# Kernel tuning notes

Measured on AMD Instinct MI355X. Metric: run time of the kernel, lower is better.

## Reference

```python
import jax, jax.numpy as jnp
import numpy as np

D = 512
M_FUT = 3
EPS = 1e-12


def _lin(x, W, b):
    return x @ W + b


def _svd_orthogonalize(m):
    # m: [B, 9] -> [B, 3, 3] SO(3) via SVD orthogonalization (special Procrustes)
    m = m.reshape(-1, 3, 3)
    norm = jnp.maximum(jnp.linalg.norm(m, axis=-1, keepdims=True), EPS)
    mt = jnp.swapaxes(m / norm, -1, -2)          # normalize rows, then transpose
    u, s, vh = jnp.linalg.svd(mt, full_matrices=False)
    v = jnp.swapaxes(vh, -1, -2)                 # torch.svd returns V, jax returns V^H
    ut = jnp.swapaxes(u, -1, -2)
    det = jnp.linalg.det(jnp.matmul(v, ut))      # [B]
    v_adj = jnp.concatenate([v[:, :, :-1], v[:, :, -1:] * det[:, None, None]], axis=2)
    return jnp.matmul(v_adj, ut)


def setup_inputs() -> dict:
    key = jax.random.key(0)
    ks = iter(jax.random.split(key, 40))
    B, N, M = 32, 3, M_FUT
    ph = pw = 37
    BN, hw = B * N, ph * pw
    sc = 1.0 / np.sqrt(D)
    rn = lambda *shape: (jax.random.normal(next(ks), shape, dtype=jnp.float32) * sc)
    inp = {
        'feat': jax.random.normal(next(ks), (BN, hw, D), dtype=jnp.float32),
        'patch_h': ph, 'patch_w': pw, 'batch_size': B, 'num_current_frames': N,
        # two ResConvBlocks, three 512x512 Linears each (in==out -> skip is identity)
        'W_res': rn(2, 3, D, D), 'b_res': rn(2, 3, D),
        # TemporalCameraMLP
        'W_cur1': rn(D, D), 'b_cur1': rn(D), 'W_cur2': rn(D, D), 'b_cur2': rn(D),
        'W_tp1': rn(D, D), 'b_tp1': rn(D), 'W_tp2': rn(D, D * M), 'b_tp2': rn(D * M),
        'W_fut1': rn(D, D), 'b_fut1': rn(D), 'W_fut2': rn(D, D), 'b_fut2': rn(D),
        # more_mlps
        'W_m1': rn(D, D), 'b_m1': rn(D), 'W_m2': rn(D, D), 'b_m2': rn(D),
        # pose heads (fp32)
        'W_t': rn(D, 3), 'b_t': rn(3), 'W_r': rn(D, 9), 'b_r': rn(9),
    }
    return inp


def reference(feat, patch_h, patch_w, batch_size, num_current_frames,
              W_res, b_res, W_cur1, b_cur1, W_cur2, b_cur2,
              W_tp1, b_tp1, W_tp2, b_tp2, W_fut1, b_fut1, W_fut2, b_fut2,
              W_m1, b_m1, W_m2, b_m2, W_t, b_t, W_r, b_r):
    B, N = batch_size, num_current_frames
    M = W_tp2.shape[1] // W_tp2.shape[0]
    # stacked residual 1x1-conv (Linear) blocks
    for i in range(2):
        x = jax.nn.relu(_lin(feat, W_res[i, 0], b_res[i, 0]))
        x = jax.nn.relu(_lin(x, W_res[i, 1], b_res[i, 1]))
        x = jax.nn.relu(_lin(x, W_res[i, 2], b_res[i, 2]))
        feat = feat + x
    # AdaptiveAvgPool2d(1) over patch grid == mean over hw
    pooled = feat.mean(axis=1)                                  # [BN, D]
    # TemporalCameraMLP
    cur = _lin(jax.nn.relu(_lin(pooled, W_cur1, b_cur1)), W_cur2, b_cur2)   # [BN, D]
    gctx = pooled.reshape(B, N, -1).mean(axis=1)                            # [B, D]
    tf = _lin(jax.nn.relu(_lin(gctx, W_tp1, b_tp1)), W_tp2, b_tp2)          # [B, D*M]
    tf = tf.reshape(B * M, -1)
    fut = _lin(jax.nn.relu(_lin(tf, W_fut1, b_fut1)), W_fut2, b_fut2)       # [B*M, D]
    allf = jnp.concatenate([cur, fut], axis=0)                              # [B*(N+M), D]
    h = jax.nn.relu(_lin(jax.nn.relu(_lin(allf, W_m1, b_m1)), W_m2, b_m2))
    # pose head in fp32
    hf = h.astype(jnp.float32)
    out_t = _lin(hf, W_t, b_t)                                  # [newBN, 3]
    out_r = _lin(hf, W_r, b_r)                                  # [newBN, 9]
    r = _svd_orthogonalize(out_r)                               # [newBN, 3, 3]
    newBN = allf.shape[0]
    pose = jnp.zeros((newBN, 4, 4), dtype=jnp.float32)
    pose = pose.at[:, :3, :3].set(r)
    pose = pose.at[:, :3, 3].set(out_t)
    pose = pose.at[:, 3, 3].set(1.0)
    return pose
```

## Files before the change

kernel.cpp:

```cpp
#include <hip/hip_runtime.h>


typedef unsigned short u16;
typedef __attribute__((ext_vector_type(8))) short short8;
typedef __attribute__((ext_vector_type(4))) float f32x4;

constexpr int  DDIM    = 512;
constexpr long R_ROWS  = 96L * 1369L;
constexpr long R_PAD   = 2054L * 64L;

__device__ __forceinline__ u16 f2b(float f) {
  union { float f; unsigned u; } x; x.f = f;
  unsigned r = (x.u + 0x7FFFu + ((x.u >> 16) & 1u)) >> 16;
  return (u16)r;
}
__device__ __forceinline__ float b2f(u16 b) {
  union { unsigned u; float f; } x; x.u = ((unsigned)b) << 16;
  return x.f;
}

__global__ void convert_feat_k(const float* __restrict__ in, u16* __restrict__ out) {
  long i4 = ((long)blockIdx.x * 256 + threadIdx.x) * 4;
  if (i4 >= R_PAD * DDIM) return;
  ushort4 o;
  if (i4 < R_ROWS * DDIM) {
    float4 v = *(const float4*)(in + i4);
    o.x = f2b(v.x); o.y = f2b(v.y); o.z = f2b(v.z); o.w = f2b(v.w);
  } else {
    o.x = 0; o.y = 0; o.z = 0; o.w = 0;
  }
  *(ushort4*)(out + i4) = o;
}

__global__ void transpose_w_k(const float* __restrict__ W, u16* __restrict__ Wt) {
  int idx = blockIdx.x * 256 + threadIdx.x;
  if (idx >= 6 * 512 * 512) return;
  int g = idx >> 18, rem = idx & 262143;
  int n = rem >> 9, k = rem & 511;
  Wt[idx] = f2b(W[(long)g * 262144 + (long)k * 512 + n]);
}

__global__ __launch_bounds__(512, 2)
void fused_res_k(u16* __restrict__ A, const u16* __restrict__ Wt3,
                 const float* __restrict__ bias3) {
  __shared__ __align__(16) u16 S[64 * 512];
  float* S32 = (float*)S;
  const int tid  = threadIdx.x;
  const int lane = tid & 63;
  const int wn   = tid >> 6;
  const int l15  = lane & 15;
  const int quad = lane >> 4;
  const long rowBase = (long)blockIdx.x * 64;

#pragma unroll
  for (int j = 0; j < 8; ++j) {
    int L = tid + 512 * j;
    int r = L >> 6, cS = L & 63;
    int c = cS ^ (r & 7);
    const u16* ga = A + (rowBase + r) * DDIM + c * 8;
    __builtin_amdgcn_global_load_lds(
        (const __attribute__((address_space(1))) void*)ga,
        (__attribute__((address_space(3))) void*)&S[L * 8], 16, 0, 0);
  }
  __syncthreads();

  for (int layer = 0; layer < 3; ++layer) {
    const u16*  W    = Wt3 + (long)layer * 262144;
    const float* bias = bias3 + layer * 512;

    f32x4 acc[4][4];
#pragma unroll
    for (int i = 0; i < 4; ++i)
#pragma unroll
      for (int j = 0; j < 4; ++j) acc[i][j] = (f32x4){0.f, 0.f, 0.f, 0.f};

    const u16* wb = W + (long)(wn * 64 + l15) * DDIM + quad * 8;
    short8 bf[4], bfN[4];
#pragma unroll
    for (int j = 0; j < 4; ++j) bf[j] = *(const short8*)(wb + j * 16 * DDIM);

#pragma unroll
    for (int kk = 0; kk < 16; ++kk) {
      if (kk < 15) {
#pragma unroll
        for (int j = 0; j < 4; ++j)
          bfN[j] = *(const short8*)(wb + j * 16 * DDIM + (kk + 1) * 32);
      }
      short8 af[4];
      const int slot = ((kk * 4 + quad) ^ (l15 & 7)) * 8;
#pragma unroll
      for (int i = 0; i < 4; ++i)
        af[i] = *(const short8*)&S[(i * 16 + l15) * DDIM + slot];
#pragma unroll
      for (int i = 0; i < 4; ++i)
#pragma unroll
        for (int j = 0; j < 4; ++j)
          acc[i][j] = __builtin_amdgcn_mfma_f32_16x16x32_bf16(af[i], bf[j], acc[i][j], 0, 0, 0);
      if (kk < 15) {
#pragma unroll
        for (int j = 0; j < 4; ++j) bf[j] = bfN[j];
      }
    }

    __syncthreads();

    float bv[4];
#pragma unroll
    for (int j = 0; j < 4; ++j) bv[j] = bias[wn * 64 + j * 16 + l15];

    if (layer < 2) {
#pragma unroll
      for (int i = 0; i < 4; ++i)
#pragma unroll
        for (int j = 0; j < 4; ++j) {
          int col = wn * 64 + j * 16 + l15;
#pragma unroll
          for (int r = 0; r < 4; ++r) {
            int row = i * 16 + quad * 4 + r;
            float v = fmaxf(acc[i][j][r] + bv[j], 0.f);
            S[row * DDIM + (((col >> 3) ^ (row & 7)) << 3) + (col & 7)] = f2b(v);
          }
        }
      __syncthreads();
    } else {
#pragma unroll
      for (int h = 0; h < 2; ++h) {
#pragma unroll
        for (int i2 = 0; i2 < 2; ++i2) {
          int i = h * 2 + i2;
#pragma unroll
          for (int j = 0; j < 4; ++j) {
            int col = wn * 64 + j * 16 + l15;
#pragma unroll
            for (int r = 0; r < 4; ++r) {
              int row = i * 16 + quad * 4 + r;
              int rl  = row - h * 32;
              float v = fmaxf(acc[i][j][r] + bv[j], 0.f);
              S32[rl * DDIM + (((col >> 2) ^ (rl & 7)) << 2) + (col & 3)] = v;
            }
          }
        }
        __syncthreads();
#pragma unroll
        for (int it = 0; it < 4; ++it) {
          int idx = it * 512 + tid;
          int r = idx >> 6, c = idx & 63;
          float4 va = *(const float4*)&S32[r * DDIM + ((((2 * c)     ^ (r & 7))) << 2)];
          float4 vb = *(const float4*)&S32[r * DDIM + ((((2 * c + 1) ^ (r & 7))) << 2)];
          long g = (rowBase + h * 32 + r) * DDIM + c * 8;
          short8 xv = *(const short8*)&A[g];
          float vv[8] = {va.x, va.y, va.z, va.w, vb.x, vb.y, vb.z, vb.w};
          short8 o;
#pragma unroll
          for (int k = 0; k < 8; ++k) o[k] = (short)f2b(vv[k] + b2f((u16)xv[k]));
          *(short8*)&A[g] = o;
        }
        __syncthreads();
      }
    }
  }
}

__global__ void zero_k(float* p, int n) {
  int i = blockIdx.x * 256 + threadIdx.x;
  if (i < n) p[i] = 0.f;
}

__global__ void pool_k(const u16* __restrict__ feat, float* __restrict__ pooled) {
  int bn = blockIdx.x, ch = blockIdx.y, d = threadIdx.x;
  int p0 = ch * 172, p1 = p0 + 172;
  if (p1 > 1369) p1 = 1369;
  float s = 0.f;
  long base = ((long)bn * 1369 + p0) * DDIM + d;
  for (int p = p0; p < p1; ++p) { s += b2f(feat[base]); base += DDIM; }
  atomicAdd(&pooled[bn * DDIM + d], s * (1.0f / 1369.0f));
}

__global__ void gctx_k(const float* __restrict__ pooled, float* __restrict__ gctx) {
  int i = blockIdx.x * 256 + threadIdx.x;
  if (i >= 32 * DDIM) return;
  int b = i >> 9, d = i & 511;
  const float* p = pooled + (long)b * 3 * DDIM + d;
  gctx[i] = (p[0] + p[DDIM] + p[2 * DDIM]) * (1.0f / 3.0f);
}

template <bool RELU>
__global__ void lin_k(const float* __restrict__ in, const float* __restrict__ W,
                      const float* __restrict__ bias, float* __restrict__ out,
                      int K, int N) {
  int n = blockIdx.x * 256 + threadIdx.x;
  int r = blockIdx.y;
  if (n >= N) return;
  float acc = bias[n];
  const float* xi = in + (long)r * K;
#pragma unroll 8
  for (int k = 0; k < K; ++k) acc = fmaf(xi[k], W[(long)k * N + n], acc);
  if (RELU) acc = fmaxf(acc, 0.f);
  out[(long)r * N + n] = acc;
}

__global__ void pose_k(const float* __restrict__ h,
                       const float* __restrict__ Wt, const float* __restrict__ bt,
                       const float* __restrict__ Wr, const float* __restrict__ br,
                       float* __restrict__ out) {
  int row = blockIdx.x;
  int lane = threadIdx.x;
  const float* hr = h + (long)row * DDIM;
  float part[12];
#pragma unroll
  for (int c = 0; c < 12; ++c) {
    float acc = 0.f;
    for (int k = lane; k < DDIM; k += 64) {
      float wvv = (c < 3) ? Wt[k * 3 + c] : Wr[k * 9 + (c - 3)];
      acc += hr[k] * wvv;
    }
#pragma unroll
    for (int off = 32; off > 0; off >>= 1) acc += __shfl_down(acc, off);
    part[c] = acc;
  }
  if (lane != 0) return;

  double t3[3];
  for (int i = 0; i < 3; ++i) t3[i] = (double)part[i] + (double)bt[i];
  double m[3][3];
  for (int i = 0; i < 3; ++i)
    for (int j = 0; j < 3; ++j) m[i][j] = (double)part[3 + i * 3 + j] + (double)br[i * 3 + j];
  for (int i = 0; i < 3; ++i) {
    double nn = sqrt(m[i][0] * m[i][0] + m[i][1] * m[i][1] + m[i][2] * m[i][2]);
    if (nn < 1e-12) nn = 1e-12;
    m[i][0] /= nn; m[i][1] /= nn; m[i][2] /= nn;
  }
  double Km[3][3];
  for (int a = 0; a < 3; ++a)
    for (int b = 0; b < 3; ++b) {
      double s = 0;
      for (int i = 0; i < 3; ++i) s += m[i][a] * m[i][b];
      Km[a][b] = s;
    }
  double V[3][3] = {{1, 0, 0}, {0, 1, 0}, {0, 0, 1}};
  const int PQ[3][2] = {{0, 1}, {0, 2}, {1, 2}};
  for (int sweep = 0; sweep < 20; ++sweep) {
    for (int e = 0; e < 3; ++e) {
      int p = PQ[e][0], q = PQ[e][1];
      double apq = Km[p][q];
      if (apq == 0.0) continue;
      double tau = (Km[q][q] - Km[p][p]) / (2.0 * apq);
      double tt = (tau >= 0.0 ? 1.0 : -1.0) / (fabs(tau) + sqrt(1.0 + tau * tau));
      double cc = 1.0 / sqrt(1.0 + tt * tt), ss = tt * cc;
      for (int k = 0; k < 3; ++k) { double a1 = Km[p][k], a2 = Km[q][k]; Km[p][k] = cc * a1 - ss * a2; Km[q][k] = ss * a1 + cc * a2; }
      for (int k = 0; k < 3; ++k) { double a1 = Km[k][p], a2 = Km[k][q]; Km[k][p] = cc * a1 - ss * a2; Km[k][q] = ss * a1 + cc * a2; }
      for (int k = 0; k < 3; ++k) { double a1 = V[k][p], a2 = V[k][q]; V[k][p] = cc * a1 - ss * a2; V[k][q] = ss * a1 + cc * a2; }
    }
  }
  double lam[3] = {Km[0][0], Km[1][1], Km[2][2]};
  int o0 = 0, o1 = 1, o2 = 2; double detV = 1.0;
  if (lam[o0] < lam[o1]) { int t = o0; o0 = o1; o1 = t; detV = -detV; }
  if (lam[o1] < lam[o2]) { int t = o1; o1 = o2; o2 = t; detV = -detV; }
  if (lam[o0] < lam[o1]) { int t = o0; o0 = o1; o1 = t; detV = -detV; }
  double v0[3] = {V[0][o0], V[1][o0], V[2][o0]};
  double v1[3] = {V[0][o1], V[1][o1], V[2][o1]};
  double v2[3] = {V[0][o2], V[1][o2], V[2][o2]};
  double u0[3], u1[3];
  for (int i = 0; i < 3; ++i) u0[i] = m[i][0] * v0[0] + m[i][1] * v0[1] + m[i][2] * v0[2];
  double n0 = sqrt(u0[0] * u0[0] + u0[1] * u0[1] + u0[2] * u0[2]); if (n0 < 1e-30) n0 = 1e-30;
  for (int i = 0; i < 3; ++i) u0[i] /= n0;
  for (int i = 0; i < 3; ++i) u1[i] = m[i][0] * v1[0] + m[i][1] * v1[1] + m[i][2] * v1[2];
  double d01 = u0[0] * u1[0] + u0[1] * u1[1] + u0[2] * u1[2];
  for (int i = 0; i < 3; ++i) u1[i] -= d01 * u0[i];
  double n1 = sqrt(u1[0] * u1[0] + u1[1] * u1[1] + u1[2] * u1[2]); if (n1 < 1e-30) n1 = 1e-30;
  for (int i = 0; i < 3; ++i) u1[i] /= n1;
  double u2[3] = {u0[1] * u1[2] - u0[2] * u1[1],
                  u0[2] * u1[0] - u0[0] * u1[2],
                  u0[0] * u1[1] - u0[1] * u1[0]};
  float* o = out + (long)row * 16;
  for (int i = 0; i < 3; ++i) {
    for (int j = 0; j < 3; ++j)
      o[i * 4 + j] = (float)(u0[i] * v0[j] + u1[i] * v1[j] + detV * u2[i] * v2[j]);
    o[i * 4 + 3] = (float)t3[i];
  }
  o[12] = 0.f; o[13] = 0.f; o[14] = 0.f; o[15] = 1.f;
}

extern "C" void kernel_launch(void* const* d_in, const int* in_sizes, int n_in,
                              void* d_out, int out_size, void* d_ws, size_t ws_size,
                              hipStream_t stream) {
  (void)in_sizes; (void)n_in; (void)out_size; (void)ws_size;
  const float* feat   = (const float*)d_in[0];
  const float* W_res  = (const float*)d_in[5];
  const float* b_res  = (const float*)d_in[6];
  const float* W_cur1 = (const float*)d_in[7];
  const float* b_cur1 = (const float*)d_in[8];
  const float* W_cur2 = (const float*)d_in[9];
  const float* b_cur2 = (const float*)d_in[10];
  const float* W_tp1  = (const float*)d_in[11];
  const float* b_tp1  = (const float*)d_in[12];
  const float* W_tp2  = (const float*)d_in[13];
  const float* b_tp2  = (const float*)d_in[14];
  const float* W_fut1 = (const float*)d_in[15];
  const float* b_fut1 = (const float*)d_in[16];
  const float* W_fut2 = (const float*)d_in[17];
  const float* b_fut2 = (const float*)d_in[18];
  const float* W_m1   = (const float*)d_in[19];
  const float* b_m1   = (const float*)d_in[20];
  const float* W_m2   = (const float*)d_in[21];
  const float* b_m2   = (const float*)d_in[22];
  const float* W_t    = (const float*)d_in[23];
  const float* b_t    = (const float*)d_in[24];
  const float* W_r    = (const float*)d_in[25];
  const float* b_r    = (const float*)d_in[26];

  char* ws = (char*)d_ws;
  const size_t SZ_BIG = (size_t)R_PAD * DDIM * 2;
  u16* A   = (u16*)(ws);
  u16* Wt6 = (u16*)(ws + 3 * SZ_BIG);
  char* tail = ws + 3 * SZ_BIG + (size_t)6 * 512 * 512 * 2;
  float* pooled = (float*)(tail);
  float* gctx   = pooled + 96 * 512;
  float* tmp    = gctx + 32 * 512;
  float* tfb    = tmp + 192 * 512;
  float* allf   = tfb + 32 * 1536;
  float* h2     = allf + 192 * 512;
  float* outp   = (float*)d_out;

  convert_feat_k<<<65728, 256, 0, stream>>>(feat, A);
  transpose_w_k<<<6144, 256, 0, stream>>>(W_res, Wt6);

  const size_t WS1 = (size_t)512 * 512;
  fused_res_k<<<2054, 512, 0, stream>>>(A, Wt6,           b_res);
  fused_res_k<<<2054, 512, 0, stream>>>(A, Wt6 + 3 * WS1, b_res + 3 * 512);

  zero_k<<<(96 * 512 + 255) / 256, 256, 0, stream>>>(pooled, 96 * 512);
  pool_k<<<dim3(96, 8), 512, 0, stream>>>(A, pooled);
  gctx_k<<<(32 * 512 + 255) / 256, 256, 0, stream>>>(pooled, gctx);

  lin_k<true ><<<dim3(2, 96),  256, 0, stream>>>(pooled, W_cur1, b_cur1, tmp, 512, 512);
  lin_k<false><<<dim3(2, 96),  256, 0, stream>>>(tmp, W_cur2, b_cur2, allf, 512, 512);
  lin_k<true ><<<dim3(2, 32),  256, 0, stream>>>(gctx, W_tp1, b_tp1, tmp, 512, 512);
  lin_k<false><<<dim3(6, 32),  256, 0, stream>>>(tmp, W_tp2, b_tp2, tfb, 512, 1536);
  lin_k<true ><<<dim3(2, 96),  256, 0, stream>>>(tfb, W_fut1, b_fut1, tmp, 512, 512);
  lin_k<false><<<dim3(2, 96),  256, 0, stream>>>(tmp, W_fut2, b_fut2, allf + 96 * 512, 512, 512);
  lin_k<true ><<<dim3(2, 192), 256, 0, stream>>>(allf, W_m1, b_m1, tmp, 512, 512);
  lin_k<true ><<<dim3(2, 192), 256, 0, stream>>>(tmp, W_m2, b_m2, h2, 512, 512);

  pose_k<<<192, 64, 0, stream>>>(h2, W_t, b_t, W_r, b_r, outp);
}
```

Measured before the change: 1.772 ms.

## Double row tile to 128 per block in fused residual GEMM kernel

Each block now processes 128 rows instead of 64, so every weight fragment loaded from global memory feeds twice as many MFMAs and total weight traffic is halved. The shared buffer grows to 128 KB with a 16-way XOR swizzle, the epilogue is reorganised into 16-row bands, and setprio is raised around the MFMA burst. The trade-off is higher register pressure from 32 accumulators and the larger LDS footprint, which likely cuts occupancy to one block per CU despite launch_bounds(512,2).

Result: slower. 2.042 ms (+15.2%).

```diff
diff --git a/kernel.cpp b/kernel.cpp
--- a/kernel.cpp
+++ b/kernel.cpp
@@ -7,7 +7,7 @@
 
 constexpr int  DDIM    = 512;
 constexpr long R_ROWS  = 96L * 1369L;
-constexpr long R_PAD   = 2054L * 64L;
+constexpr long R_PAD   = 1027L * 128L;
 
 __device__ __forceinline__ u16 f2b(float f) {
   union { float f; unsigned u; } x; x.f = f;
@@ -17,6 +17,10 @@
 __device__ __forceinline__ float b2f(u16 b) {
   union { unsigned u; float f; } x; x.u = ((unsigned)b) << 16;
   return x.f;
+}
+__device__ __forceinline__ int swzf(int m) {
+  m &= 15;
+  return (m ^ (m >> 3)) & 15;
 }
 
 __global__ void convert_feat_k(const float* __restrict__ in, u16* __restrict__ out) {
@@ -43,20 +47,20 @@
 __global__ __launch_bounds__(512, 2)
 void fused_res_k(u16* __restrict__ A, const u16* __restrict__ Wt3,
                  const float* __restrict__ bias3) {
-  __shared__ __align__(16) u16 S[64 * 512];
+  __shared__ __align__(16) u16 S[128 * 512];
   float* S32 = (float*)S;
   const int tid  = threadIdx.x;
   const int lane = tid & 63;
   const int wn   = tid >> 6;
   const int l15  = lane & 15;
   const int quad = lane >> 4;
-  const long rowBase = (long)blockIdx.x * 64;
-
-#pragma unroll
-  for (int j = 0; j < 8; ++j) {
+  const long rowBase = (long)blockIdx.x * 128;
+
+#pragma unroll
+  for (int j = 0; j < 16; ++j) {
     int L = tid + 512 * j;
     int r = L >> 6, cS = L & 63;
-    int c = cS ^ (r & 7);
+    int c = cS ^ swzf(r);
     const u16* ga = A + (rowBase + r) * DDIM + c * 8;
     __builtin_amdgcn_global_load_lds(
         (const __attribute__((address_space(1))) void*)ga,
@@ -68,9 +72,9 @@
     const u16*  W    = Wt3 + (long)layer * 262144;
     const float* bias = bias3 + layer * 512;
 
-    f32x4 acc[4][4];
-#pragma unroll
-    for (int i = 0; i < 4; ++i)
+    f32x4 acc[8][4];
+#pragma unroll
+    for (int i = 0; i < 8; ++i)
 #pragma unroll
       for (int j = 0; j < 4; ++j) acc[i][j] = (f32x4){0.f, 0.f, 0.f, 0.f};
 
@@ -86,16 +90,18 @@
         for (int j = 0; j < 4; ++j)
           bfN[j] = *(const short8*)(wb + j * 16 * DDIM + (kk + 1) * 32);
       }
-      short8 af[4];
-      const int slot = ((kk * 4 + quad) ^ (l15 & 7)) * 8;
-#pragma unroll
-      for (int i = 0; i < 4; ++i)
+      short8 af[8];
+      const int slot = ((kk * 4 + quad) ^ swzf(l15)) * 8;
+#pragma unroll
+      for (int i = 0; i < 8; ++i)
         af[i] = *(const short8*)&S[(i * 16 + l15) * DDIM + slot];
-#pragma unroll
-      for (int i = 0; i < 4; ++i)
+      __builtin_amdgcn_s_setprio(1);
+#pragma unroll
+      for (int i = 0; i < 8; ++i)
 #pragma unroll
         for (int j = 0; j < 4; ++j)
           acc[i][j] = __builtin_amdgcn_mfma_f32_16x16x32_bf16(af[i], bf[j], acc[i][j], 0, 0, 0);
+      __builtin_amdgcn_s_setprio(0);
       if (kk < 15) {
 #pragma unroll
         for (int j = 0; j < 4; ++j) bf[j] = bfN[j];
@@ -110,7 +116,7 @@
 
     if (layer < 2) {
 #pragma unroll
-      for (int i = 0; i < 4; ++i)
+      for (int i = 0; i < 8; ++i)
 #pragma unroll
         for (int j = 0; j < 4; ++j) {
           int col = wn * 64 + j * 16 + l15;
@@ -118,42 +124,40 @@
           for (int r = 0; r < 4; ++r) {
             int row = i * 16 + quad * 4 + r;
             float v = fmaxf(acc[i][j][r] + bv[j], 0.f);
-            S[row * DDIM + (((col >> 3) ^ (row & 7)) << 3) + (col & 7)] = f2b(v);
+            S[row * DDIM + ((((col >> 3) ^ swzf(row)) << 3) | (col & 7))] = f2b(v);
           }
         }
       __syncthreads();
     } else {
 #pragma unroll
-      for (int h = 0; h < 2; ++h) {
-#pragma unroll
-        for (int i2 = 0; i2 < 2; ++i2) {
-          int i = h * 2 + i2;
-#pragma unroll
-          for (int j = 0; j < 4; ++j) {
-            int col = wn * 64 + j * 16 + l15;
-#pragma unroll
-            for (int r = 0; r < 4; ++r) {
-              int row = i * 16 + quad * 4 + r;
-              int rl  = row - h * 32;
-              float v = fmaxf(acc[i][j][r] + bv[j], 0.f);
-              S32[rl * DDIM + (((col >> 2) ^ (rl & 7)) << 2) + (col & 3)] = v;
-            }
+      for (int band = 0; band < 8; ++band) {
+#pragma unroll
+        for (int j = 0; j < 4; ++j) {
+          int col = wn * 64 + j * 16 + l15;
+#pragma unroll
+          for (int r = 0; r < 4; ++r) {
+            int rl = quad * 4 + r;
+            float v = fmaxf(acc[band][j][r] + bv[j], 0.f);
+            S32[rl * 512 + ((((col >> 2) ^ swzf(rl)) << 2) | (col & 3))] = v;
           }
         }
         __syncthreads();
-#pragma unroll
-        for (int it = 0; it < 4; ++it) {
-          int idx = it * 512 + tid;
-          int r = idx >> 6, c = idx & 63;
-          float4 va = *(const float4*)&S32[r * DDIM + ((((2 * c)     ^ (r & 7))) << 2)];
-          float4 vb = *(const float4*)&S32[r * DDIM + ((((2 * c + 1) ^ (r & 7))) << 2)];
-          long g = (rowBase + h * 32 + r) * DDIM + c * 8;
-          short8 xv = *(const short8*)&A[g];
-          float vv[8] = {va.x, va.y, va.z, va.w, vb.x, vb.y, vb.z, vb.w};
-          short8 o;
-#pragma unroll
-          for (int k = 0; k < 8; ++k) o[k] = (short)f2b(vv[k] + b2f((u16)xv[k]));
-          *(short8*)&A[g] = o;
+        {
+          int rl = tid >> 5, a = tid & 31;
+          float v[16];
+#pragma unroll
+          for (int q = 0; q < 4; ++q)
+            *(float4*)&v[q * 4] = *(const float4*)&S32[rl * 512 + ((((a * 4 + q) ^ swzf(rl)) << 2))];
+          long g = (rowBase + band * 16 + rl) * DDIM + a * 16;
+          short8 x0 = *(const short8*)&A[g];
+          short8 x1 = *(const short8*)&A[g + 8];
+          short8 o0, o1;
+#pragma unroll
+          for (int k = 0; k < 8; ++k) o0[k] = (short)f2b(v[k] + b2f((u16)x0[k]));
+#pragma unroll
+          for (int k = 0; k < 8; ++k) o1[k] = (short)f2b(v[8 + k] + b2f((u16)x1[k]));
+          *(short8*)&A[g] = o0;
+          *(short8*)&A[g + 8] = o1;
         }
         __syncthreads();
       }
@@ -326,8 +330,8 @@
   transpose_w_k<<<6144, 256, 0, stream>>>(W_res, Wt6);
 
   const size_t WS1 = (size_t)512 * 512;
-  fused_res_k<<<2054, 512, 0, stream>>>(A, Wt6,           b_res);
-  fused_res_k<<<2054, 512, 0, stream>>>(A, Wt6 + 3 * WS1, b_res + 3 * 512);
+  fused_res_k<<<1027, 512, 0, stream>>>(A, Wt6,           b_res);
+  fused_res_k<<<1027, 512, 0, stream>>>(A, Wt6 + 3 * WS1, b_res + 3 * 512);
 
   zero_k<<<(96 * 512 + 255) / 256, 256, 0, stream>>>(pooled, 96 * 512);
   pool_k<<<dim3(96, 8), 512, 0, stream>>>(A, pooled);
```
